# Kernel optimization log

Measured on AMD Instinct MI355X. Metric: run time of the kernel, lower is better.

## Reference

```python
import jax, jax.numpy as jnp
import numpy as np


def setup_inputs() -> dict:
    key = jax.random.key(0)
    k1, k2 = jax.random.split(key)
    inputs = jax.random.normal(k1, (4096, 2048), dtype=jnp.float32)
    targets = jax.random.randint(k2, (4096,), 0, 64, dtype=jnp.int64)
    return {"inputs": inputs, "targets": targets}


def reference(inputs, targets):
    n = inputs.shape[0]
    # pairwise Euclidean distances: ||xi||^2 + ||xj||^2 - 2 xi.xj, clamped + sqrt
    sq = jnp.sum(inputs * inputs, axis=1)  # [n]
    dist2 = sq[:, None] + sq[None, :] - 2.0 * (inputs @ inputs.T)
    dist = jnp.sqrt(jnp.maximum(dist2, 1e-12))  # [n, n]
    mask = targets[:, None] == targets[None, :]  # same-class mask, diag True
    # farthest positive per row
    far = jnp.max(jnp.where(mask, dist, -jnp.inf), axis=1)  # [n]
    # second-nearest positive per row (nearest is self, dist=1e-6)
    neg_masked = jnp.where(mask, -dist, -jnp.inf)
    top2, _ = jax.lax.top_k(neg_masked, 2)  # two smallest distances (negated)
    near = -top2[:, 1]  # [n]
    # MarginRankingLoss(margin=0), y=1: mean(max(0, -(near - far)))
    return jnp.mean(jax.nn.relu(far - near))
```

## Files before the change

### kernel.cpp

```cpp
#include <hip/hip_runtime.h>
#include <hip/hip_bf16.h>
#include <cstdint>
#include <cstddef>

#define N_PTS 4096
#define DIM   2048
#define NCLS  64
#define NKG   4
#define CHUNK 256
#define MAXT  2

typedef __bf16 bf16x8 __attribute__((ext_vector_type(8)));
typedef float  f32x4  __attribute__((ext_vector_type(4)));

__device__ __forceinline__ unsigned short f32_to_bf16_rne(float f) {
  unsigned u = __float_as_uint(f);
  u += 0x7fffu + ((u >> 16) & 1u);
  return (unsigned short)(u >> 16);
}
__device__ __forceinline__ int imin(int a, int b) { return a < b ? a : b; }

__device__ __forceinline__ int scan_class(const int* __restrict__ tgt, int c,
                                          int* idx_tmp, int* idx_sh, int* cnt_s) {
  const int tid = threadIdx.x;
  if (tid == 0) *cnt_s = 0;
  __syncthreads();
  #pragma unroll
  for (int r = 0; r < 8; ++r) {
    const int i = r * 512 + tid;
    if (tgt[i] == c) {
      int p = atomicAdd(cnt_s, 1);
      if (p < 128) idx_tmp[p] = i;
    }
  }
  __syncthreads();
  int n = *cnt_s; if (n > 128) n = 128;
  if (n <= 0) return 0;
  if (tid < n) {
    const int mine = idx_tmp[tid];
    int rank = 0;
    for (int j = 0; j < n; ++j) rank += (idx_tmp[j] < mine);
    idx_sh[rank] = mine;
  }
  __syncthreads();
  if (tid < 128 && tid >= n) idx_sh[tid] = idx_sh[n - 1];
  __syncthreads();
  return n;
}

__global__ __launch_bounds__(512) void gram_kernel(
    const float* __restrict__ X, const int* __restrict__ tgt,
    float* __restrict__ Gpart, float* __restrict__ out) {
  const int c = blockIdx.x >> 2, kg = blockIdx.x & 3;
  __shared__ __align__(16) char sm[65536];
  __shared__ int idx_tmp[128], idx_sh[128], cnt_s;

  const int tid = threadIdx.x;
  if (blockIdx.x == 0 && tid == 0) out[0] = 0.0f;

  const int n = scan_class(tgt, c, idx_tmp, idx_sh, &cnt_s);
  if (n <= 0) return;
  int T = (n + 63) >> 6; if (T > MAXT) T = MAXT;

  const int lane = tid & 63, w = tid >> 6;
  const int fr = lane & 15, hi4 = lane >> 4;
  const int srow8 = tid >> 3, sc = tid & 7;
  const int ard = (fr << 6) + ((hi4 << 4) ^ ((lane & 8) << 2));

  const float* src0 = X + (size_t)idx_sh[srow8] * DIM + kg * 512;
  const float* src1 = X + (size_t)idx_sh[64 + srow8] * DIM + kg * 512;

  float4 v0[8], v1[8];
#define LOADR(s_) do { \
    const float4* p0_ = (const float4*)(src0 + (s_) * CHUNK); \
    _Pragma("unroll") for (int it = 0; it < 8; ++it) v0[it] = p0_[sc + it * 8]; \
    if (T == 2) { \
      const float4* p1_ = (const float4*)(src1 + (s_) * CHUNK); \
      _Pragma("unroll") for (int it = 0; it < 8; ++it) v1[it] = p1_[sc + it * 8]; \
    } } while (0)

#define WROW(vv, rr) do { \
    _Pragma("unroll") for (int it = 0; it < 8; ++it) { \
      const int col = (sc + it * 8) * 4; \
      ushort4 o; \
      o.x = f32_to_bf16_rne(vv[it].x); o.y = f32_to_bf16_rne(vv[it].y); \
      o.z = f32_to_bf16_rne(vv[it].z); o.w = f32_to_bf16_rne(vv[it].w); \
      const int byte = ((((rr) >> 4) * 8 + (col >> 5)) << 10) + (((rr) & 15) << 6) \
                     + (((col & 31) << 1) ^ (((rr) & 8) << 2)); \
      *(ushort4*)(sm + byte) = o; \
    } } while (0)

  f32x4 acc[2][4] = {};
  const int mp = w & 3, nq = w >> 2;
  const int m1 = w >> 1, nn0 = (w & 1) * 2;

#define COMPUTE() do { \
    if (T == 2) { \
      _Pragma("unroll") for (int kk = 0; kk < 8; ++kk) { \
        bf16x8 a0 = *(const bf16x8*)(sm + (((mp * 2    ) * 8 + kk) << 10) + ard); \
        bf16x8 a1 = *(const bf16x8*)(sm + (((mp * 2 + 1) * 8 + kk) << 10) + ard); \
        _Pragma("unroll") for (int j = 0; j < 4; ++j) { \
          bf16x8 b = *(const bf16x8*)(sm + (((nq * 4 + j) * 8 + kk) << 10) + ard); \
          acc[0][j] = __builtin_amdgcn_mfma_f32_16x16x32_bf16(a0, b, acc[0][j], 0, 0, 0); \
          acc[1][j] = __builtin_amdgcn_mfma_f32_16x16x32_bf16(a1, b, acc[1][j], 0, 0, 0); \
        } \
      } \
    } else { \
      _Pragma("unroll") for (int kk = 0; kk < 8; ++kk) { \
        bf16x8 a  = *(const bf16x8*)(sm + ((m1 * 8 + kk) << 10) + ard); \
        bf16x8 b0 = *(const bf16x8*)(sm + (((nn0    ) * 8 + kk) << 10) + ard); \
        bf16x8 b1 = *(const bf16x8*)(sm + (((nn0 + 1) * 8 + kk) << 10) + ard); \
        acc[0][0] = __builtin_amdgcn_mfma_f32_16x16x32_bf16(a, b0, acc[0][0], 0, 0, 0); \
        acc[0][1] = __builtin_amdgcn_mfma_f32_16x16x32_bf16(a, b1, acc[0][1], 0, 0, 0); \
      } \
    } } while (0)

  LOADR(0);
  WROW(v0, srow8);
  if (T == 2) WROW(v1, 64 + srow8);
  __syncthreads();
  LOADR(1);
  COMPUTE();
  __syncthreads();
  WROW(v0, srow8);
  if (T == 2) WROW(v1, 64 + srow8);
  __syncthreads();
  COMPUTE();
#undef LOADR
#undef WROW
#undef COMPUTE

  if (T == 2) {
    #pragma unroll
    for (int i = 0; i < 2; ++i)
      #pragma unroll
      for (int j = 0; j < 4; ++j) {
        const int fm = mp * 2 + i, fn = nq * 4 + j;
        const int u = (fm >> 2) * 2 + (fn >> 2);
        float* gd = Gpart + ((((size_t)c * 4 + u) * 4 + kg) << 12);
        const int r0 = (fm & 3) * 16 + hi4 * 4, c0 = (fn & 3) * 16 + fr;
        #pragma unroll
        for (int r = 0; r < 4; ++r) gd[(r0 + r) * 64 + c0] = acc[i][j][r];
      }
  } else {
    float* gd = Gpart + (((size_t)c * 4 * 4 + kg) << 12);
    const int r0 = m1 * 16 + hi4 * 4;
    #pragma unroll
    for (int j = 0; j < 2; ++j)
      #pragma unroll
      for (int r = 0; r < 4; ++r)
        gd[(r0 + r) * 64 + (nn0 + j) * 16 + fr] = acc[0][j][r];
  }
}

__global__ __launch_bounds__(512) void combine_kernel(
    const float* __restrict__ Gpart, const int* __restrict__ tgt,
    float* __restrict__ out) {
  const int c = blockIdx.x >> 1, rt = blockIdx.x & 1;
  __shared__ int cnt_s;
  __shared__ float diag[MAXT * 64];
  __shared__ float red[512];
  const int tid = threadIdx.x, lane = tid & 63;

  if (tid == 0) cnt_s = 0;
  __syncthreads();
  int local = 0;
  #pragma unroll
  for (int r = 0; r < 8; ++r) local += (tgt[r * 512 + tid] == c) ? 1 : 0;
  #pragma unroll
  for (int off = 32; off > 0; off >>= 1) local += __shfl_down(local, off, 64);
  if (lane == 0) atomicAdd(&cnt_s, local);
  __syncthreads();
  const int n = imin(cnt_s, 128);
  if (n <= 0) return;
  int T = (n + 63) >> 6; if (T > MAXT) T = MAXT;
  if (rt >= T) return;
  const float* gc = Gpart + ((size_t)c << 16);

  for (int j = tid; j < T * 64; j += 512) {
    const int jt = j >> 6, jp = j & 63;
    const float* gu = gc + (((size_t)(jt * 3) * 4) << 12) + jp * 65;
    float s = 0.0f;
    #pragma unroll
    for (int k = 0; k < 4; ++k) s += gu[k << 12];
    diag[j] = s;
  }
  __syncthreads();

  const int rsub = tid >> 3, cq = tid & 7;
  const float INF = __builtin_inff();
  const int row = rt * 64 + rsub;
  const float di = diag[row];
  float fmx = 0.0f, nmn = INF;
  for (int ct = 0; ct < T; ++ct) {
    const float* gu = gc + (((size_t)(rt * 2 + ct) * 4) << 12) + rsub * 64 + cq * 8;
    f32x4 g0 = {}, g1 = {};
    #pragma unroll
    for (int k = 0; k < 4; ++k) {
      g0 += *(const f32x4*)(gu + (k << 12));
      g1 += *(const f32x4*)(gu + (k << 12) + 4);
    }
    #pragma unroll
    for (int i = 0; i < 8; ++i) {
      const int col = ct * 64 + cq * 8 + i;
      const float gv = (i < 4) ? g0[i] : g1[i - 4];
      if (col < n) {
        const float d2 = fmaf(-2.0f, gv, di + diag[col]);
        fmx = fmaxf(fmx, d2);
        if (col != row) nmn = fminf(nmn, d2);
      }
    }
  }
  fmx = fmaxf(fmx, __shfl_xor(fmx, 1, 64)); nmn = fminf(nmn, __shfl_xor(nmn, 1, 64));
  fmx = fmaxf(fmx, __shfl_xor(fmx, 2, 64)); nmn = fminf(nmn, __shfl_xor(nmn, 2, 64));
  fmx = fmaxf(fmx, __shfl_xor(fmx, 4, 64)); nmn = fminf(nmn, __shfl_xor(nmn, 4, 64));

  float contrib = 0.0f;
  if (cq == 0 && row < n) {
    const float fa = sqrtf(fmaxf(fmx, 1e-12f));
    const float ne = sqrtf(fmaxf(nmn, 1e-12f));
    contrib = fmaxf(fa - ne, 0.0f);
  }
  red[tid] = contrib;
  __syncthreads();
  for (int off = 256; off > 0; off >>= 1) {
    if (tid < off) red[tid] += red[tid + off];
    __syncthreads();
  }
  if (tid == 0) atomicAdd(out, red[0] * (1.0f / (float)N_PTS));
}

extern "C" void kernel_launch(void* const* d_in, const int* in_sizes, int n_in,
                              void* d_out, int out_size, void* d_ws, size_t ws_size,
                              hipStream_t stream) {
  const float* X   = (const float*)d_in[0];
  const int*   tgt = (const int*)d_in[1];
  float*       out = (float*)d_out;

  float* Gpart = (float*)d_ws;

  gram_kernel<<<NCLS * NKG, 512, 0, stream>>>(X, tgt, Gpart, out);
  combine_kernel<<<NCLS * MAXT, 512, 0, stream>>>(Gpart, tgt, out);
}
```

Baseline: 23.92 us.

## Fuse gram and combine kernels into one per-class block with LDS reduction

Measured after the change: 36.42 us. +52.3%, slower.

```diff
diff --git a/kernel.cpp b/kernel.cpp
--- a/kernel.cpp
+++ b/kernel.cpp
@@ -6,9 +6,10 @@
 #define N_PTS 4096
 #define DIM   2048
 #define NCLS  64
-#define NKG   4
 #define CHUNK 256
+#define NSUB  8
 #define MAXT  2
+#define GSTR  132
 
 typedef __bf16 bf16x8 __attribute__((ext_vector_type(8)));
 typedef float  f32x4  __attribute__((ext_vector_type(4)));
@@ -20,22 +21,31 @@
 }
 __device__ __forceinline__ int imin(int a, int b) { return a < b ? a : b; }
 
-__device__ __forceinline__ int scan_class(const int* __restrict__ tgt, int c,
-                                          int* idx_tmp, int* idx_sh, int* cnt_s) {
+__global__ __launch_bounds__(512) void fused_kernel(
+    const float* __restrict__ X, const int* __restrict__ tgt,
+    float* __restrict__ out) {
+  const int c = blockIdx.x;
+  __shared__ __align__(16) char sm[69632];
+  __shared__ int idx_tmp[128], idx_sh[128];
+  __shared__ int cnt_s;
+  __shared__ float diag[128];
+  __shared__ float red[512];
+
   const int tid = threadIdx.x;
-  if (tid == 0) *cnt_s = 0;
+
+  if (tid == 0) cnt_s = 0;
   __syncthreads();
   #pragma unroll
   for (int r = 0; r < 8; ++r) {
     const int i = r * 512 + tid;
     if (tgt[i] == c) {
-      int p = atomicAdd(cnt_s, 1);
+      int p = atomicAdd(&cnt_s, 1);
       if (p < 128) idx_tmp[p] = i;
     }
   }
   __syncthreads();
-  int n = *cnt_s; if (n > 128) n = 128;
-  if (n <= 0) return 0;
+  int n = cnt_s; if (n > 128) n = 128;
+  if (n <= 0) return;
   if (tid < n) {
     const int mine = idx_tmp[tid];
     int rank = 0;
@@ -45,30 +55,16 @@
   __syncthreads();
   if (tid < 128 && tid >= n) idx_sh[tid] = idx_sh[n - 1];
   __syncthreads();
-  return n;
-}
-
-__global__ __launch_bounds__(512) void gram_kernel(
-    const float* __restrict__ X, const int* __restrict__ tgt,
-    float* __restrict__ Gpart, float* __restrict__ out) {
-  const int c = blockIdx.x >> 2, kg = blockIdx.x & 3;
-  __shared__ __align__(16) char sm[65536];
-  __shared__ int idx_tmp[128], idx_sh[128], cnt_s;
-
-  const int tid = threadIdx.x;
-  if (blockIdx.x == 0 && tid == 0) out[0] = 0.0f;
-
-  const int n = scan_class(tgt, c, idx_tmp, idx_sh, &cnt_s);
-  if (n <= 0) return;
-  int T = (n + 63) >> 6; if (T > MAXT) T = MAXT;
+  const int T = imin((n + 63) >> 6, MAXT);
+  const int P = T * 64;
 
   const int lane = tid & 63, w = tid >> 6;
   const int fr = lane & 15, hi4 = lane >> 4;
   const int srow8 = tid >> 3, sc = tid & 7;
   const int ard = (fr << 6) + ((hi4 << 4) ^ ((lane & 8) << 2));
 
-  const float* src0 = X + (size_t)idx_sh[srow8] * DIM + kg * 512;
-  const float* src1 = X + (size_t)idx_sh[64 + srow8] * DIM + kg * 512;
+  const float* src0 = X + (size_t)idx_sh[srow8] * DIM;
+  const float* src1 = X + (size_t)idx_sh[64 + srow8] * DIM;
 
   float4 v0[8], v1[8];
 #define LOADR(s_) do { \
@@ -116,110 +112,71 @@
     } } while (0)
 
   LOADR(0);
-  WROW(v0, srow8);
-  if (T == 2) WROW(v1, 64 + srow8);
-  __syncthreads();
-  LOADR(1);
-  COMPUTE();
-  __syncthreads();
-  WROW(v0, srow8);
-  if (T == 2) WROW(v1, 64 + srow8);
-  __syncthreads();
-  COMPUTE();
+  for (int s = 0; s < NSUB; ++s) {
+    WROW(v0, srow8);
+    if (T == 2) WROW(v1, 64 + srow8);
+    __syncthreads();
+    if (s + 1 < NSUB) LOADR(s + 1);
+    COMPUTE();
+    __syncthreads();
+  }
 #undef LOADR
 #undef WROW
 #undef COMPUTE
 
+  float* G = (float*)sm;
   if (T == 2) {
     #pragma unroll
     for (int i = 0; i < 2; ++i)
       #pragma unroll
       for (int j = 0; j < 4; ++j) {
         const int fm = mp * 2 + i, fn = nq * 4 + j;
-        const int u = (fm >> 2) * 2 + (fn >> 2);
-        float* gd = Gpart + ((((size_t)c * 4 + u) * 4 + kg) << 12);
-        const int r0 = (fm & 3) * 16 + hi4 * 4, c0 = (fn & 3) * 16 + fr;
+        const int r0 = fm * 16 + hi4 * 4, c0 = fn * 16 + fr;
         #pragma unroll
-        for (int r = 0; r < 4; ++r) gd[(r0 + r) * 64 + c0] = acc[i][j][r];
+        for (int r = 0; r < 4; ++r) G[(r0 + r) * GSTR + c0] = acc[i][j][r];
       }
   } else {
-    float* gd = Gpart + (((size_t)c * 4 * 4 + kg) << 12);
     const int r0 = m1 * 16 + hi4 * 4;
     #pragma unroll
     for (int j = 0; j < 2; ++j)
       #pragma unroll
       for (int r = 0; r < 4; ++r)
-        gd[(r0 + r) * 64 + (nn0 + j) * 16 + fr] = acc[0][j][r];
+        G[(r0 + r) * GSTR + (nn0 + j) * 16 + fr] = acc[0][j][r];
   }
-}
-
-__global__ __launch_bounds__(512) void combine_kernel(
-    const float* __restrict__ Gpart, const int* __restrict__ tgt,
-    float* __restrict__ out) {
-  const int c = blockIdx.x >> 1, rt = blockIdx.x & 1;
-  __shared__ int cnt_s;
-  __shared__ float diag[MAXT * 64];
-  __shared__ float red[512];
-  const int tid = threadIdx.x, lane = tid & 63;
-
-  if (tid == 0) cnt_s = 0;
   __syncthreads();
-  int local = 0;
-  #pragma unroll
-  for (int r = 0; r < 8; ++r) local += (tgt[r * 512 + tid] == c) ? 1 : 0;
-  #pragma unroll
-  for (int off = 32; off > 0; off >>= 1) local += __shfl_down(local, off, 64);
-  if (lane == 0) atomicAdd(&cnt_s, local);
-  __syncthreads();
-  const int n = imin(cnt_s, 128);
-  if (n <= 0) return;
-  int T = (n + 63) >> 6; if (T > MAXT) T = MAXT;
-  if (rt >= T) return;
-  const float* gc = Gpart + ((size_t)c << 16);
-
-  for (int j = tid; j < T * 64; j += 512) {
-    const int jt = j >> 6, jp = j & 63;
-    const float* gu = gc + (((size_t)(jt * 3) * 4) << 12) + jp * 65;
-    float s = 0.0f;
-    #pragma unroll
-    for (int k = 0; k < 4; ++k) s += gu[k << 12];
-    diag[j] = s;
-  }
+  for (int j = tid; j < P; j += 512) diag[j] = G[j * (GSTR + 1)];
   __syncthreads();
 
   const int rsub = tid >> 3, cq = tid & 7;
+  const int npc = P >> 3;
   const float INF = __builtin_inff();
-  const int row = rt * 64 + rsub;
-  const float di = diag[row];
-  float fmx = 0.0f, nmn = INF;
-  for (int ct = 0; ct < T; ++ct) {
-    const float* gu = gc + (((size_t)(rt * 2 + ct) * 4) << 12) + rsub * 64 + cq * 8;
-    f32x4 g0 = {}, g1 = {};
-    #pragma unroll
-    for (int k = 0; k < 4; ++k) {
-      g0 += *(const f32x4*)(gu + (k << 12));
-      g1 += *(const f32x4*)(gu + (k << 12) + 4);
-    }
-    #pragma unroll
-    for (int i = 0; i < 8; ++i) {
-      const int col = ct * 64 + cq * 8 + i;
-      const float gv = (i < 4) ? g0[i] : g1[i - 4];
-      if (col < n) {
-        const float d2 = fmaf(-2.0f, gv, di + diag[col]);
-        fmx = fmaxf(fmx, d2);
-        if (col != row) nmn = fminf(nmn, d2);
+  float contrib = 0.0f;
+  for (int rt = 0; rt < T; ++rt) {
+    const int row = rt * 64 + rsub;
+    float fmx = 0.0f, nmn = INF;
+    if (row < n) {
+      const float di = diag[row];
+      const float* gr = G + row * GSTR + cq * npc;
+      #pragma unroll
+      for (int i = 0; i < 16; ++i) {
+        if (i < npc) {
+          const int col = cq * npc + i;
+          if (col < n) {
+            const float d2 = fmaf(-2.0f, gr[i], di + diag[col]);
+            fmx = fmaxf(fmx, d2);
+            if (col != row) nmn = fminf(nmn, d2);
+          }
+        }
       }
     }
-  }
-  fmx = fmaxf(fmx, __shfl_xor(fmx, 1, 64)); nmn = fminf(nmn, __shfl_xor(nmn, 1, 64));
-  fmx = fmaxf(fmx, __shfl_xor(fmx, 2, 64)); nmn = fminf(nmn, __shfl_xor(nmn, 2, 64));
-  fmx = fmaxf(fmx, __shfl_xor(fmx, 4, 64)); nmn = fminf(nmn, __shfl_xor(nmn, 4, 64));
-
-  float contrib = 0.0f;
-  if (cq == 0 && row < n) {
-    const float fa = sqrtf(fmaxf(fmx, 1e-12f));
-    const float ne = sqrtf(fmaxf(nmn, 1e-12f));
-    contrib = fmaxf(fa - ne, 0.0f);
+    fmx = fmaxf(fmx, __shfl_xor(fmx, 1, 64)); nmn = fminf(nmn, __shfl_xor(nmn, 1, 64));
+    fmx = fmaxf(fmx, __shfl_xor(fmx, 2, 64)); nmn = fminf(nmn, __shfl_xor(nmn, 2, 64));
+    fmx = fmaxf(fmx, __shfl_xor(fmx, 4, 64)); nmn = fminf(nmn, __shfl_xor(nmn, 4, 64));
+    if (cq == 0 && row < n) {
+      const float fa = sqrtf(fmaxf(fmx, 1e-12f));
+      const float ne = sqrtf(fmaxf(nmn, 1e-12f));
+      contrib += fmaxf(fa - ne, 0.0f);
+    }
   }
   red[tid] = contrib;
   __syncthreads();
@@ -237,8 +194,6 @@
   const int*   tgt = (const int*)d_in[1];
   float*       out = (float*)d_out;
 
-  float* Gpart = (float*)d_ws;
-
-  gram_kernel<<<NCLS * NKG, 512, 0, stream>>>(X, tgt, Gpart, out);
-  combine_kernel<<<NCLS * MAXT, 512, 0, stream>>>(Gpart, tgt, out);
+  hipMemsetAsync(out, 0, sizeof(float), stream);
+  fused_kernel<<<NCLS, 512, 0, stream>>>(X, tgt, out);
 }
```

## Fuse gram and combine kernels into one cooperative launch with grid sync

Applied to the files above, without the earlier changes.

Measured after the change: 76.51 us. +219.9%, slower.

```diff
diff --git a/kernel.cpp b/kernel.cpp
--- a/kernel.cpp
+++ b/kernel.cpp
@@ -1,4 +1,5 @@
 #include <hip/hip_runtime.h>
+#include <hip/hip_cooperative_groups.h>
 #include <hip/hip_bf16.h>
 #include <cstdint>
 #include <cstddef>
@@ -10,6 +11,8 @@
 #define CHUNK 256
 #define MAXT  2
 
+namespace cg = cooperative_groups;
+
 typedef __bf16 bf16x8 __attribute__((ext_vector_type(8)));
 typedef float  f32x4  __attribute__((ext_vector_type(4)));
 
@@ -20,63 +23,63 @@
 }
 __device__ __forceinline__ int imin(int a, int b) { return a < b ? a : b; }
 
-__device__ __forceinline__ int scan_class(const int* __restrict__ tgt, int c,
-                                          int* idx_tmp, int* idx_sh, int* cnt_s) {
-  const int tid = threadIdx.x;
-  if (tid == 0) *cnt_s = 0;
-  __syncthreads();
-  #pragma unroll
-  for (int r = 0; r < 8; ++r) {
-    const int i = r * 512 + tid;
-    if (tgt[i] == c) {
-      int p = atomicAdd(cnt_s, 1);
-      if (p < 128) idx_tmp[p] = i;
-    }
-  }
-  __syncthreads();
-  int n = *cnt_s; if (n > 128) n = 128;
-  if (n <= 0) return 0;
-  if (tid < n) {
-    const int mine = idx_tmp[tid];
-    int rank = 0;
-    for (int j = 0; j < n; ++j) rank += (idx_tmp[j] < mine);
-    idx_sh[rank] = mine;
-  }
-  __syncthreads();
-  if (tid < 128 && tid >= n) idx_sh[tid] = idx_sh[n - 1];
-  __syncthreads();
-  return n;
-}
-
-__global__ __launch_bounds__(512) void gram_kernel(
+__global__ __launch_bounds__(512) void fused_kernel(
     const float* __restrict__ X, const int* __restrict__ tgt,
     float* __restrict__ Gpart, float* __restrict__ out) {
-  const int c = blockIdx.x >> 2, kg = blockIdx.x & 3;
   __shared__ __align__(16) char sm[65536];
   __shared__ int idx_tmp[128], idx_sh[128], cnt_s;
+  __shared__ float diag[MAXT * 64];
+  __shared__ float red[512];
 
   const int tid = threadIdx.x;
-  if (blockIdx.x == 0 && tid == 0) out[0] = 0.0f;
-
-  const int n = scan_class(tgt, c, idx_tmp, idx_sh, &cnt_s);
-  if (n <= 0) return;
-  int T = (n + 63) >> 6; if (T > MAXT) T = MAXT;
-
   const int lane = tid & 63, w = tid >> 6;
-  const int fr = lane & 15, hi4 = lane >> 4;
-  const int srow8 = tid >> 3, sc = tid & 7;
-  const int ard = (fr << 6) + ((hi4 << 4) ^ ((lane & 8) << 2));
-
-  const float* src0 = X + (size_t)idx_sh[srow8] * DIM + kg * 512;
-  const float* src1 = X + (size_t)idx_sh[64 + srow8] * DIM + kg * 512;
-
-  float4 v0[8], v1[8];
+
+  {
+    const int c = blockIdx.x >> 2, kg = blockIdx.x & 3;
+
+    if (tid == 0) cnt_s = 0;
+    __syncthreads();
+    #pragma unroll
+    for (int r = 0; r < 8; ++r) {
+      const int i = r * 512 + tid;
+      if (tgt[i] == c) {
+        int p = atomicAdd(&cnt_s, 1);
+        if (p < 128) idx_tmp[p] = i;
+      }
+    }
+    __syncthreads();
+    int n = cnt_s; if (n > 128) n = 128;
+    if (n > 0) {
+      if (tid < n) {
+        const int mine = idx_tmp[tid];
+        int rank = 0;
+        for (int j = 0; j < n; ++j) rank += (idx_tmp[j] < mine);
+        idx_sh[rank] = mine;
+      }
+      __syncthreads();
+      if (tid < 128 && tid >= n) idx_sh[tid] = idx_sh[n - 1];
+      __syncthreads();
+      const int T = imin((n + 63) >> 6, MAXT);
+
+      const int fr = lane & 15, hi4 = lane >> 4;
+      const int srow8 = tid >> 3, sc = tid & 7;
+      const int ard = (fr << 6) + ((hi4 << 4) ^ ((lane & 8) << 2));
+      const bool real0 = (srow8 < n);
+      const bool real1 = (64 + srow8 < n);
+
+      const float* src0 = X + (size_t)idx_sh[srow8] * DIM + kg * 512;
+      const float* src1 = X + (size_t)idx_sh[64 + srow8] * DIM + kg * 512;
+      const float4 f4z = {0.f, 0.f, 0.f, 0.f};
+
+      float4 v0[8], v1[8];
 #define LOADR(s_) do { \
-    const float4* p0_ = (const float4*)(src0 + (s_) * CHUNK); \
-    _Pragma("unroll") for (int it = 0; it < 8; ++it) v0[it] = p0_[sc + it * 8]; \
+    if (real0) { const float4* p0_ = (const float4*)(src0 + (s_) * CHUNK); \
+      _Pragma("unroll") for (int it = 0; it < 8; ++it) v0[it] = p0_[sc + it * 8]; \
+    } else { _Pragma("unroll") for (int it = 0; it < 8; ++it) v0[it] = f4z; } \
     if (T == 2) { \
-      const float4* p1_ = (const float4*)(src1 + (s_) * CHUNK); \
-      _Pragma("unroll") for (int it = 0; it < 8; ++it) v1[it] = p1_[sc + it * 8]; \
+      if (real1) { const float4* p1_ = (const float4*)(src1 + (s_) * CHUNK); \
+        _Pragma("unroll") for (int it = 0; it < 8; ++it) v1[it] = p1_[sc + it * 8]; \
+      } else { _Pragma("unroll") for (int it = 0; it < 8; ++it) v1[it] = f4z; } \
     } } while (0)
 
 #define WROW(vv, rr) do { \
@@ -90,9 +93,9 @@
       *(ushort4*)(sm + byte) = o; \
     } } while (0)
 
-  f32x4 acc[2][4] = {};
-  const int mp = w & 3, nq = w >> 2;
-  const int m1 = w >> 1, nn0 = (w & 1) * 2;
+      f32x4 acc[2][4] = {};
+      const int mp = w & 3, nq = w >> 2;
+      const int m1 = w >> 1, nn0 = (w & 1) * 2;
 
 #define COMPUTE() do { \
     if (T == 2) { \
@@ -115,119 +118,116 @@
       } \
     } } while (0)
 
-  LOADR(0);
-  WROW(v0, srow8);
-  if (T == 2) WROW(v1, 64 + srow8);
-  __syncthreads();
-  LOADR(1);
-  COMPUTE();
-  __syncthreads();
-  WROW(v0, srow8);
-  if (T == 2) WROW(v1, 64 + srow8);
-  __syncthreads();
-  COMPUTE();
+      LOADR(0);
+      WROW(v0, srow8);
+      if (T == 2) WROW(v1, 64 + srow8);
+      __syncthreads();
+      LOADR(1);
+      COMPUTE();
+      __syncthreads();
+      WROW(v0, srow8);
+      if (T == 2) WROW(v1, 64 + srow8);
+      __syncthreads();
+      COMPUTE();
 #undef LOADR
 #undef WROW
 #undef COMPUTE
 
-  if (T == 2) {
+      if (T == 2) {
+        #pragma unroll
+        for (int i = 0; i < 2; ++i)
+          #pragma unroll
+          for (int j = 0; j < 4; ++j) {
+            const int fm = mp * 2 + i, fn = nq * 4 + j;
+            const int u = (fm >> 2) * 2 + (fn >> 2);
+            float* gd = Gpart + ((((size_t)c * 4 + u) * 4 + kg) << 12);
+            const int r0 = (fm & 3) * 16 + hi4 * 4, c0 = (fn & 3) * 16 + fr;
+            #pragma unroll
+            for (int r = 0; r < 4; ++r) gd[(r0 + r) * 64 + c0] = acc[i][j][r];
+          }
+      } else {
+        float* gd = Gpart + (((size_t)c * 4 * 4 + kg) << 12);
+        const int r0 = m1 * 16 + hi4 * 4;
+        #pragma unroll
+        for (int j = 0; j < 2; ++j)
+          #pragma unroll
+          for (int r = 0; r < 4; ++r)
+            gd[(r0 + r) * 64 + (nn0 + j) * 16 + fr] = acc[0][j][r];
+      }
+    }
+  }
+
+  cg::this_grid().sync();
+
+  if (blockIdx.x < NCLS * MAXT) {
+    const int c = blockIdx.x >> 1, rt = blockIdx.x & 1;
+    if (tid == 0) cnt_s = 0;
+    __syncthreads();
+    int local = 0;
     #pragma unroll
-    for (int i = 0; i < 2; ++i)
+    for (int r = 0; r < 8; ++r) local += (tgt[r * 512 + tid] == c) ? 1 : 0;
+    #pragma unroll
+    for (int off = 32; off > 0; off >>= 1) local += __shfl_down(local, off, 64);
+    if (lane == 0) atomicAdd(&cnt_s, local);
+    __syncthreads();
+    const int n = imin(cnt_s, 128);
+    if (n <= 0) return;
+    int T = (n + 63) >> 6; if (T > MAXT) T = MAXT;
+    if (rt >= T) return;
+    const float* gc = Gpart + ((size_t)c << 16);
+
+    for (int j = tid; j < T * 64; j += 512) {
+      const int jt = j >> 6, jp = j & 63;
+      const float* gu = gc + (((size_t)(jt * 3) * 4) << 12) + jp * 65;
+      float s = 0.0f;
       #pragma unroll
-      for (int j = 0; j < 4; ++j) {
-        const int fm = mp * 2 + i, fn = nq * 4 + j;
-        const int u = (fm >> 2) * 2 + (fn >> 2);
-        float* gd = Gpart + ((((size_t)c * 4 + u) * 4 + kg) << 12);
-        const int r0 = (fm & 3) * 16 + hi4 * 4, c0 = (fn & 3) * 16 + fr;
-        #pragma unroll
-        for (int r = 0; r < 4; ++r) gd[(r0 + r) * 64 + c0] = acc[i][j][r];
-      }
-  } else {
-    float* gd = Gpart + (((size_t)c * 4 * 4 + kg) << 12);
-    const int r0 = m1 * 16 + hi4 * 4;
-    #pragma unroll
-    for (int j = 0; j < 2; ++j)
+      for (int k = 0; k < 4; ++k) s += gu[k << 12];
+      diag[j] = s;
+    }
+    __syncthreads();
+
+    const int rsub = tid >> 3, cq = tid & 7;
+    const float INF = __builtin_inff();
+    const int row = rt * 64 + rsub;
+    const float di = diag[row];
+    float fmx = 0.0f, nmn = INF;
+    for (int ct = 0; ct < T; ++ct) {
+      const float* gu = gc + (((size_t)(rt * 2 + ct) * 4) << 12) + rsub * 64 + cq * 8;
+      f32x4 g0 = {}, g1 = {};
       #pragma unroll
-      for (int r = 0; r < 4; ++r)
-        gd[(r0 + r) * 64 + (nn0 + j) * 16 + fr] = acc[0][j][r];
+      for (int k = 0; k < 4; ++k) {
+        g0 += *(const f32x4*)(gu + (k << 12));
+        g1 += *(const f32x4*)(gu + (k << 12) + 4);
+      }
+      #pragma unroll
+      for (int i = 0; i < 8; ++i) {
+        const int col = ct * 64 + cq * 8 + i;
+        const float gv = (i < 4) ? g0[i] : g1[i - 4];
+        if (col < n) {
+          const float d2 = fmaf(-2.0f, gv, di + diag[col]);
+          fmx = fmaxf(fmx, d2);
+          if (col != row) nmn = fminf(nmn, d2);
+        }
+      }
+    }
+    fmx = fmaxf(fmx, __shfl_xor(fmx, 1, 64)); nmn = fminf(nmn, __shfl_xor(nmn, 1, 64));
+    fmx = fmaxf(fmx, __shfl_xor(fmx, 2, 64)); nmn = fminf(nmn, __shfl_xor(nmn, 2, 64));
+    fmx = fmaxf(fmx, __shfl_xor(fmx, 4, 64)); nmn = fminf(nmn, __shfl_xor(nmn, 4, 64));
+
+    float contrib = 0.0f;
+    if (cq == 0 && row < n) {
+      const float fa = sqrtf(fmaxf(fmx, 1e-12f));
+      const float ne = sqrtf(fmaxf(nmn, 1e-12f));
+      contrib = fmaxf(fa - ne, 0.0f);
+    }
+    red[tid] = contrib;
+    __syncthreads();
+    for (int off = 256; off > 0; off >>= 1) {
+      if (tid < off) red[tid] += red[tid + off];
+      __syncthreads();
+    }
+    if (tid == 0) atomicAdd(out, red[0] * (1.0f / (float)N_PTS));
   }
-}
-
-__global__ __launch_bounds__(512) void combine_kernel(
-    const float* __restrict__ Gpart, const int* __restrict__ tgt,
-    float* __restrict__ out) {
-  const int c = blockIdx.x >> 1, rt = blockIdx.x & 1;
-  __shared__ int cnt_s;
-  __shared__ float diag[MAXT * 64];
-  __shared__ float red[512];
-  const int tid = threadIdx.x, lane = tid & 63;
-
-  if (tid == 0) cnt_s = 0;
-  __syncthreads();
-  int local = 0;
-  #pragma unroll
-  for (int r = 0; r < 8; ++r) local += (tgt[r * 512 + tid] == c) ? 1 : 0;
-  #pragma unroll
-  for (int off = 32; off > 0; off >>= 1) local += __shfl_down(local, off, 64);
-  if (lane == 0) atomicAdd(&cnt_s, local);
-  __syncthreads();
-  const int n = imin(cnt_s, 128);
-  if (n <= 0) return;
-  int T = (n + 63) >> 6; if (T > MAXT) T = MAXT;
-  if (rt >= T) return;
-  const float* gc = Gpart + ((size_t)c << 16);
-
-  for (int j = tid; j < T * 64; j += 512) {
-    const int jt = j >> 6, jp = j & 63;
-    const float* gu = gc + (((size_t)(jt * 3) * 4) << 12) + jp * 65;
-    float s = 0.0f;
-    #pragma unroll
-    for (int k = 0; k < 4; ++k) s += gu[k << 12];
-    diag[j] = s;
-  }
-  __syncthreads();
-
-  const int rsub = tid >> 3, cq = tid & 7;
-  const float INF = __builtin_inff();
-  const int row = rt * 64 + rsub;
-  const float di = diag[row];
-  float fmx = 0.0f, nmn = INF;
-  for (int ct = 0; ct < T; ++ct) {
-    const float* gu = gc + (((size_t)(rt * 2 + ct) * 4) << 12) + rsub * 64 + cq * 8;
-    f32x4 g0 = {}, g1 = {};
-    #pragma unroll
-    for (int k = 0; k < 4; ++k) {
-      g0 += *(const f32x4*)(gu + (k << 12));
-      g1 += *(const f32x4*)(gu + (k << 12) + 4);
-    }
-    #pragma unroll
-    for (int i = 0; i < 8; ++i) {
-      const int col = ct * 64 + cq * 8 + i;
-      const float gv = (i < 4) ? g0[i] : g1[i - 4];
-      if (col < n) {
-        const float d2 = fmaf(-2.0f, gv, di + diag[col]);
-        fmx = fmaxf(fmx, d2);
-        if (col != row) nmn = fminf(nmn, d2);
-      }
-    }
-  }
-  fmx = fmaxf(fmx, __shfl_xor(fmx, 1, 64)); nmn = fminf(nmn, __shfl_xor(nmn, 1, 64));
-  fmx = fmaxf(fmx, __shfl_xor(fmx, 2, 64)); nmn = fminf(nmn, __shfl_xor(nmn, 2, 64));
-  fmx = fmaxf(fmx, __shfl_xor(fmx, 4, 64)); nmn = fminf(nmn, __shfl_xor(nmn, 4, 64));
-
-  float contrib = 0.0f;
-  if (cq == 0 && row < n) {
-    const float fa = sqrtf(fmaxf(fmx, 1e-12f));
-    const float ne = sqrtf(fmaxf(nmn, 1e-12f));
-    contrib = fmaxf(fa - ne, 0.0f);
-  }
-  red[tid] = contrib;
-  __syncthreads();
-  for (int off = 256; off > 0; off >>= 1) {
-    if (tid < off) red[tid] += red[tid + off];
-    __syncthreads();
-  }
-  if (tid == 0) atomicAdd(out, red[0] * (1.0f / (float)N_PTS));
 }
 
 extern "C" void kernel_launch(void* const* d_in, const int* in_sizes, int n_in,
@@ -236,9 +236,11 @@
   const float* X   = (const float*)d_in[0];
   const int*   tgt = (const int*)d_in[1];
   float*       out = (float*)d_out;
-
-  float* Gpart = (float*)d_ws;
-
-  gram_kernel<<<NCLS * NKG, 512, 0, stream>>>(X, tgt, Gpart, out);
-  combine_kernel<<<NCLS * MAXT, 512, 0, stream>>>(Gpart, tgt, out);
+  float*       Gpart = (float*)d_ws;
+
+  hipMemsetAsync(out, 0, sizeof(float), stream);
+
+  void* args[] = {(void*)&X, (void*)&tgt, (void*)&Gpart, (void*)&out};
+  hipLaunchCooperativeKernel((const void*)fused_kernel,
+                             dim3(NCLS * NKG), dim3(512), args, 0, stream);
 }
```

## Use ballot-based class scan, skip padded row loads, larger per-wave MFMA tiles

Applied to the files above, without the earlier changes.

After: 23.67 us, median of 2. Within noise of the previous version (-1.0%).

```diff
diff --git a/kernel.cpp b/kernel.cpp
--- a/kernel.cpp
+++ b/kernel.cpp
@@ -20,63 +20,70 @@
 }
 __device__ __forceinline__ int imin(int a, int b) { return a < b ? a : b; }
 
-__device__ __forceinline__ int scan_class(const int* __restrict__ tgt, int c,
-                                          int* idx_tmp, int* idx_sh, int* cnt_s) {
-  const int tid = threadIdx.x;
-  if (tid == 0) *cnt_s = 0;
-  __syncthreads();
-  #pragma unroll
-  for (int r = 0; r < 8; ++r) {
-    const int i = r * 512 + tid;
-    if (tgt[i] == c) {
-      int p = atomicAdd(cnt_s, 1);
-      if (p < 128) idx_tmp[p] = i;
-    }
-  }
-  __syncthreads();
-  int n = *cnt_s; if (n > 128) n = 128;
-  if (n <= 0) return 0;
-  if (tid < n) {
-    const int mine = idx_tmp[tid];
-    int rank = 0;
-    for (int j = 0; j < n; ++j) rank += (idx_tmp[j] < mine);
-    idx_sh[rank] = mine;
-  }
-  __syncthreads();
-  if (tid < 128 && tid >= n) idx_sh[tid] = idx_sh[n - 1];
-  __syncthreads();
-  return n;
-}
-
 __global__ __launch_bounds__(512) void gram_kernel(
     const float* __restrict__ X, const int* __restrict__ tgt,
     float* __restrict__ Gpart, float* __restrict__ out) {
   const int c = blockIdx.x >> 2, kg = blockIdx.x & 3;
   __shared__ __align__(16) char sm[65536];
-  __shared__ int idx_tmp[128], idx_sh[128], cnt_s;
+  __shared__ int idx_sh[128];
+  __shared__ int cnts[64], offs[64];
+  __shared__ int n_sh;
 
   const int tid = threadIdx.x;
+  const int lane = tid & 63, w = tid >> 6;
   if (blockIdx.x == 0 && tid == 0) out[0] = 0.0f;
 
-  const int n = scan_class(tgt, c, idx_tmp, idx_sh, &cnt_s);
+  unsigned long long msk[8];
+  #pragma unroll
+  for (int r = 0; r < 8; ++r)
+    msk[r] = __ballot(tgt[r * 512 + tid] == c);
+  if (lane == 0) {
+    #pragma unroll
+    for (int r = 0; r < 8; ++r) cnts[r * 8 + w] = (int)__popcll(msk[r]);
+  }
+  __syncthreads();
+  if (tid == 0) {
+    int run = 0;
+    for (int o = 0; o < 64; ++o) { offs[o] = run; run += cnts[o]; }
+    n_sh = run;
+  }
+  __syncthreads();
+  int n = n_sh; if (n > 128) n = 128;
   if (n <= 0) return;
-  int T = (n + 63) >> 6; if (T > MAXT) T = MAXT;
-
-  const int lane = tid & 63, w = tid >> 6;
+  {
+    const unsigned long long lt = (lane == 0) ? 0ull : ((~0ull) >> (64 - lane));
+    #pragma unroll
+    for (int r = 0; r < 8; ++r) {
+      if ((msk[r] >> lane) & 1ull) {
+        const int rank = offs[r * 8 + w] + (int)__popcll(msk[r] & lt);
+        if (rank < 128) idx_sh[rank] = r * 512 + tid;
+      }
+    }
+  }
+  __syncthreads();
+  if (tid < 128 && tid >= n) idx_sh[tid] = idx_sh[n - 1];
+  __syncthreads();
+  const int T = imin((n + 63) >> 6, MAXT);
+
   const int fr = lane & 15, hi4 = lane >> 4;
   const int srow8 = tid >> 3, sc = tid & 7;
   const int ard = (fr << 6) + ((hi4 << 4) ^ ((lane & 8) << 2));
+  const bool real0 = (srow8 < n);
+  const bool real1 = (64 + srow8 < n);
 
   const float* src0 = X + (size_t)idx_sh[srow8] * DIM + kg * 512;
   const float* src1 = X + (size_t)idx_sh[64 + srow8] * DIM + kg * 512;
+  const float4 f4z = {0.f, 0.f, 0.f, 0.f};
 
   float4 v0[8], v1[8];
 #define LOADR(s_) do { \
-    const float4* p0_ = (const float4*)(src0 + (s_) * CHUNK); \
-    _Pragma("unroll") for (int it = 0; it < 8; ++it) v0[it] = p0_[sc + it * 8]; \
+    if (real0) { const float4* p0_ = (const float4*)(src0 + (s_) * CHUNK); \
+      _Pragma("unroll") for (int it = 0; it < 8; ++it) v0[it] = p0_[sc + it * 8]; \
+    } else { _Pragma("unroll") for (int it = 0; it < 8; ++it) v0[it] = f4z; } \
     if (T == 2) { \
-      const float4* p1_ = (const float4*)(src1 + (s_) * CHUNK); \
-      _Pragma("unroll") for (int it = 0; it < 8; ++it) v1[it] = p1_[sc + it * 8]; \
+      if (real1) { const float4* p1_ = (const float4*)(src1 + (s_) * CHUNK); \
+        _Pragma("unroll") for (int it = 0; it < 8; ++it) v1[it] = p1_[sc + it * 8]; \
+      } else { _Pragma("unroll") for (int it = 0; it < 8; ++it) v1[it] = f4z; } \
     } } while (0)
 
 #define WROW(vv, rr) do { \
@@ -90,28 +97,23 @@
       *(ushort4*)(sm + byte) = o; \
     } } while (0)
 
-  f32x4 acc[2][4] = {};
-  const int mp = w & 3, nq = w >> 2;
-  const int m1 = w >> 1, nn0 = (w & 1) * 2;
+  f32x4 acc[4][4] = {};
+  const int mq = w >> 1, nq = w & 1;
+  const bool comp = (T == 2) ? (w < 4) : (w == 0);
+  const int aoff = (T == 2) ? mq * 4 : 0;
+  const int boff = (T == 2) ? nq * 4 : 0;
 
 #define COMPUTE() do { \
-    if (T == 2) { \
+    if (comp) { \
       _Pragma("unroll") for (int kk = 0; kk < 8; ++kk) { \
-        bf16x8 a0 = *(const bf16x8*)(sm + (((mp * 2    ) * 8 + kk) << 10) + ard); \
-        bf16x8 a1 = *(const bf16x8*)(sm + (((mp * 2 + 1) * 8 + kk) << 10) + ard); \
-        _Pragma("unroll") for (int j = 0; j < 4; ++j) { \
-          bf16x8 b = *(const bf16x8*)(sm + (((nq * 4 + j) * 8 + kk) << 10) + ard); \
-          acc[0][j] = __builtin_amdgcn_mfma_f32_16x16x32_bf16(a0, b, acc[0][j], 0, 0, 0); \
-          acc[1][j] = __builtin_amdgcn_mfma_f32_16x16x32_bf16(a1, b, acc[1][j], 0, 0, 0); \
+        bf16x8 a[4], b[4]; \
+        _Pragma("unroll") for (int i = 0; i < 4; ++i) { \
+          a[i] = *(const bf16x8*)(sm + (((aoff + i) * 8 + kk) << 10) + ard); \
+          b[i] = *(const bf16x8*)(sm + (((boff + i) * 8 + kk) << 10) + ard); \
         } \
-      } \
-    } else { \
-      _Pragma("unroll") for (int kk = 0; kk < 8; ++kk) { \
-        bf16x8 a  = *(const bf16x8*)(sm + ((m1 * 8 + kk) << 10) + ard); \
-        bf16x8 b0 = *(const bf16x8*)(sm + (((nn0    ) * 8 + kk) << 10) + ard); \
-        bf16x8 b1 = *(const bf16x8*)(sm + (((nn0 + 1) * 8 + kk) << 10) + ard); \
-        acc[0][0] = __builtin_amdgcn_mfma_f32_16x16x32_bf16(a, b0, acc[0][0], 0, 0, 0); \
-        acc[0][1] = __builtin_amdgcn_mfma_f32_16x16x32_bf16(a, b1, acc[0][1], 0, 0, 0); \
+        _Pragma("unroll") for (int i = 0; i < 4; ++i) \
+          _Pragma("unroll") for (int j = 0; j < 4; ++j) \
+            acc[i][j] = __builtin_amdgcn_mfma_f32_16x16x32_bf16(a[i], b[j], acc[i][j], 0, 0, 0); \
       } \
     } } while (0)
 
@@ -130,26 +132,17 @@
 #undef WROW
 #undef COMPUTE
 
-  if (T == 2) {
-    #pragma unroll
-    for (int i = 0; i < 2; ++i)
+  if (comp) {
+    const int u = (T == 2) ? (mq * 2 + nq) : 0;
+    float* gd = Gpart + ((((size_t)c * 4 + u) * 4 + kg) << 12);
+    #pragma unroll
+    for (int i = 0; i < 4; ++i)
       #pragma unroll
       for (int j = 0; j < 4; ++j) {
-        const int fm = mp * 2 + i, fn = nq * 4 + j;
-        const int u = (fm >> 2) * 2 + (fn >> 2);
-        float* gd = Gpart + ((((size_t)c * 4 + u) * 4 + kg) << 12);
-        const int r0 = (fm & 3) * 16 + hi4 * 4, c0 = (fn & 3) * 16 + fr;
+        const int r0 = i * 16 + hi4 * 4, c0 = j * 16 + fr;
         #pragma unroll
         for (int r = 0; r < 4; ++r) gd[(r0 + r) * 64 + c0] = acc[i][j][r];
       }
-  } else {
-    float* gd = Gpart + (((size_t)c * 4 * 4 + kg) << 12);
-    const int r0 = m1 * 16 + hi4 * 4;
-    #pragma unroll
-    for (int j = 0; j < 2; ++j)
-      #pragma unroll
-      for (int r = 0; r < 4; ++r)
-        gd[(r0 + r) * 64 + (nn0 + j) * 16 + fr] = acc[0][j][r];
   }
 }
 
```
